# Kernel tuning notes

Hardware: AMD Instinct MI355X
Metric: run time of the kernel (lower is better)

## Reference

```python
import jax, jax.numpy as jnp
import numpy as np

B, T, D = 2, 2048, 1024
NH, DH = 16, 64
DD_PAIRS = DH // 4          # 16
DD_DIM = DD_PAIRS * 2      # 32
FFN = (D * 8 // 3 + 7) // 8 * 8  # 2736
EPS = 1e-6


def rms_norm(x, w):
    # torch nn.RMSNorm: x / sqrt(mean(x^2) + eps) * w over last dim
    var = jnp.mean(jnp.square(x), axis=-1, keepdims=True)
    return x * jax.lax.rsqrt(var + EPS) * w


def apply_rotary(x, cos, sin):
    d = x.shape[-1]
    x1, x2 = x[..., : d // 2], x[..., d // 2 :]
    return jnp.concatenate([x1 * cos - x2 * sin, x2 * cos + x1 * sin], axis=-1)


def setup_inputs() -> dict:
    key = jax.random.key(0)
    ks = jax.random.split(key, 10)
    s = 0.02  # small init scale so activations stay sane
    # fixed RoPE tables: (1, T, 1, DH//2)
    inv_freq = 1.0 / (10000.0 ** (jnp.arange(DH // 2, dtype=jnp.float32) / (DH // 2)))
    ang = jnp.arange(T, dtype=jnp.float32)[:, None] * inv_freq[None, :]  # (T, 32)
    rope_cos = jnp.cos(ang)[None, :, None, :]
    rope_sin = jnp.sin(ang)[None, :, None, :]
    return {
        "x": jax.random.normal(ks[0], (B, T, D), jnp.float32),
        "rope_cos": rope_cos,
        "rope_sin": rope_sin,
        "lerp_w": jax.random.normal(ks[1], (D, D), jnp.float32) * s,
        "lerp_b": jnp.full((D,), -2.0, jnp.float32),
        "attn_norm_w": jnp.ones((D,), jnp.float32),
        "w_qkv": jax.random.normal(ks[2], (3 * D, D), jnp.float32) * s,
        "q_norm_w": jnp.ones((DH,), jnp.float32),
        "k_norm_w": jnp.ones((DH,), jnp.float32),
        "q_post_bias": jnp.ones((DH,), jnp.float32),
        "k_post_bias": jnp.ones((DH,), jnp.float32),
        "dd_w": jax.random.normal(ks[3], (NH * DD_PAIRS, D), jnp.float32) * s,
        "dd_b": jnp.zeros((NH * DD_PAIRS,), jnp.float32),
        "w_o": jax.random.normal(ks[4], (D, D), jnp.float32) * s,
        "mlp_norm_w": jnp.ones((D,), jnp.float32),
        "gate_w": jax.random.normal(ks[5], (FFN, D), jnp.float32) * s,
        "up_w": jax.random.normal(ks[6], (FFN, D), jnp.float32) * s,
        "down_w": jax.random.normal(ks[7], (D, FFN), jnp.float32) * s,
    }


def reference(x, rope_cos, rope_sin, lerp_w, lerp_b, attn_norm_w, w_qkv,
              q_norm_w, k_norm_w, q_post_bias, k_post_bias, dd_w, dd_b,
              w_o, mlp_norm_w, gate_w, up_w, down_w):
    # CausalLerp: x[t] <- (1-g)*x[t] + g*x[t-1], content-gated
    x_prev = jnp.pad(x[:, :-1], ((0, 0), (1, 0), (0, 0)))
    g = jax.nn.sigmoid(x @ lerp_w.T + lerp_b)
    x = (1.0 - g) * x + g * x_prev

    # Attention branch
    h = rms_norm(x, attn_norm_w)
    qkv = (h @ w_qkv.T).reshape(B, T, 3, NH, DH)
    q, k, v = qkv[:, :, 0], qkv[:, :, 1], qkv[:, :, 2]  # (B,T,NH,DH)
    q = rms_norm(q, q_norm_w) * q_post_bias
    k = rms_norm(k, k_norm_w) * k_post_bias

    # DD-RoPE angles: cumsum of learned deltas over time
    dd_angles = (x @ dd_w.T + dd_b).reshape(B, T, NH, DD_PAIRS)
    dd_angles = jnp.cumsum(dd_angles, axis=1)
    dd_cos, dd_sin = jnp.cos(dd_angles), jnp.sin(dd_angles)

    fp = DD_DIM // 2  # 16
    def hybrid(qk):
        fixed = apply_rotary(qk[..., :DD_DIM], rope_cos[..., :fp], rope_sin[..., :fp])
        dd = apply_rotary(qk[..., DD_DIM:], dd_cos, dd_sin)
        return jnp.concatenate([fixed, dd], axis=-1)

    q, k = hybrid(q), hybrid(k)

    # causal SDPA
    scale = 1.0 / jnp.sqrt(jnp.float32(DH))
    scores = jnp.einsum("bihd,bjhd->bhij", q, k) * scale  # (B,NH,T,T)
    causal = jnp.tril(jnp.ones((T, T), bool))
    scores = jnp.where(causal, scores, jnp.float32(-1e30))
    attn = jax.nn.softmax(scores, axis=-1)
    y = jnp.einsum("bhij,bjhd->bihd", attn, v).reshape(B, T, D)
    x = x + y @ w_o.T

    # SwiGLU MLP
    h = rms_norm(x, mlp_norm_w)
    x = x + (jax.nn.silu(h @ gate_w.T) * (h @ up_w.T)) @ down_w.T
    return x
```

## Files before the change

### kernel.cpp

```cpp
#include <hip/hip_runtime.h>

typedef unsigned short u16;
typedef __attribute__((ext_vector_type(8))) short short8;
typedef __attribute__((ext_vector_type(4))) float f32x4;
typedef __attribute__((ext_vector_type(4))) unsigned short u16x4;

static constexpr int TB   = 2;
static constexpr int TT   = 2048;
static constexpr int TD   = 1024;
static constexpr int TNH  = 16;
static constexpr int TDH  = 64;
static constexpr int TFFN = 2736;
static constexpr int TFFNP= 2752;
static constexpr int TBT  = TB * TT;

#define DEVI static __device__ __forceinline__

typedef __attribute__((address_space(1))) const unsigned int gas_t;
typedef __attribute__((address_space(3))) unsigned int las_t;
#define GLOAD16(src, dst) __builtin_amdgcn_global_load_lds((gas_t*)(src), (las_t*)(dst), 16, 0, 0)

DEVI u16 f2bf(float f) {
  union { float f; unsigned u; } v; v.f = f;
  unsigned r = v.u + 0x7FFFu + ((v.u >> 16) & 1u);
  return (u16)(r >> 16);
}
DEVI float bf2f(u16 u) {
  union { unsigned u; float f; } v; v.u = ((unsigned)u) << 16;
  return v.f;
}

__global__ void k_cvt(const float* __restrict__ s, u16* __restrict__ d, int n4) {
  int i = blockIdx.x * blockDim.x + threadIdx.x;
  int st = gridDim.x * blockDim.x;
  for (; i < n4; i += st) {
    float4 v = ((const float4*)s)[i];
    u16x4 u;
    u.x = f2bf(v.x); u.y = f2bf(v.y); u.z = f2bf(v.z); u.w = f2bf(v.w);
    ((u16x4*)d)[i] = u;
  }
}

__global__ void k_cvt_split(const float* __restrict__ s, u16* __restrict__ hi,
                            u16* __restrict__ lo, int n) {
  int i = blockIdx.x * blockDim.x + threadIdx.x;
  int st = gridDim.x * blockDim.x;
  for (; i < n; i += st) {
    float v = s[i];
    u16 h = f2bf(v);
    hi[i] = h;
    lo[i] = f2bf(v - bf2f(h));
  }
}

__global__ void k_cvt_pad(const float* __restrict__ s, u16* __restrict__ d,
                          int rows, int scol, int dcol) {
  int i = blockIdx.x * blockDim.x + threadIdx.x;
  int st = gridDim.x * blockDim.x;
  int n = rows * dcol;
  for (; i < n; i += st) {
    int c = i % dcol, r = i / dcol;
    d[i] = (c < scol) ? f2bf(s[(size_t)r * scol + c]) : (u16)0;
  }
}

__global__ __launch_bounds__(256) void k_rmsnorm(const float* __restrict__ x,
                                                 const float* __restrict__ w,
                                                 u16* __restrict__ o) {
  int row = blockIdx.x;
  float4 v = ((const float4*)(x + (size_t)row * TD))[threadIdx.x];
  float ss = v.x*v.x + v.y*v.y + v.z*v.z + v.w*v.w;
  #pragma unroll
  for (int m = 1; m < 64; m <<= 1) ss += __shfl_xor(ss, m);
  __shared__ float red[4];
  if ((threadIdx.x & 63) == 0) red[threadIdx.x >> 6] = ss;
  __syncthreads();
  float tot = red[0] + red[1] + red[2] + red[3];
  float sc = rsqrtf(tot * (1.0f / TD) + 1e-6f);
  float4 wv = ((const float4*)w)[threadIdx.x];
  u16x4 u;
  u.x = f2bf(v.x * sc * wv.x); u.y = f2bf(v.y * sc * wv.y);
  u.z = f2bf(v.z * sc * wv.z); u.w = f2bf(v.w * sc * wv.w);
  ((u16x4*)(o + (size_t)row * TD))[threadIdx.x] = u;
}

enum { EPI_LERP = 0, EPI_DD = 1, EPI_RESID = 2, EPI_B16 = 3 };

template<int EPI>
__global__ __launch_bounds__(256) void k_gemm_p4(
    const u16* __restrict__ A, const u16* __restrict__ B,
    int M, int N, int K,
    const float* __restrict__ aux0, const float* __restrict__ aux1,
    float* __restrict__ outF, u16* __restrict__ outB) {
  alignas(16) __shared__ u16 As[4][4096];
  alignas(16) __shared__ u16 Bs[4][4096];
  const int lane = threadIdx.x & 63;
  const int w  = threadIdx.x >> 6;
  const int ln = lane & 15;
  const int g  = lane >> 4;
  const int swz = (ln >> 1) & 3;
  const int m0 = blockIdx.x * 128;
  const int n0 = blockIdx.y * 128;
  const int wm = (w >> 1) * 64;
  const int wn = (w & 1) * 64;

  const f32x4 fz = {0.f, 0.f, 0.f, 0.f};
  f32x4 acc[4][4];
  #pragma unroll
  for (int mi = 0; mi < 4; mi++)
    #pragma unroll
    for (int ni = 0; ni < 4; ni++) acc[mi][ni] = fz;

  const int rsub = lane >> 2;
  const int csrc = (lane & 3) ^ ((lane >> 3) & 3);
  auto stage = [&](int buf, int kt) {
    const int k0 = kt * 32 + csrc * 8;
    #pragma unroll
    for (int i = 0; i < 2; i++) {
      const int u = w + i * 4;
      int ar = m0 + u * 16 + rsub;
      GLOAD16(A + (size_t)ar * K + k0, &As[buf][u * 512]);
      int br = n0 + u * 16 + rsub; if (br > N - 1) br = N - 1;
      GLOAD16(B + (size_t)br * K + k0, &Bs[buf][u * 512]);
    }
  };

  const int nt = K / 32;
  stage(0, 0);
  stage(1, 1);
  for (int t = 0; t < nt; ++t) {
    const int cur = t & 3;
    if (t + 2 < nt) {
      stage((t + 2) & 3, t + 2);
      asm volatile("s_waitcnt vmcnt(8)" ::: "memory");
    } else if (t + 1 < nt) {
      asm volatile("s_waitcnt vmcnt(4)" ::: "memory");
    } else {
      asm volatile("s_waitcnt vmcnt(0)" ::: "memory");
    }
    __builtin_amdgcn_s_barrier();
    asm volatile("" ::: "memory");

    short8 af[4], bfr[4];
    #pragma unroll
    for (int mi = 0; mi < 4; mi++)
      af[mi] = *(const short8*)&As[cur][(wm + mi * 16 + ln) * 32 + ((g ^ swz) << 3)];
    #pragma unroll
    for (int ni = 0; ni < 4; ni++)
      bfr[ni] = *(const short8*)&Bs[cur][(wn + ni * 16 + ln) * 32 + ((g ^ swz) << 3)];
    #pragma unroll
    for (int mi = 0; mi < 4; mi++)
      #pragma unroll
      for (int ni = 0; ni < 4; ni++)
        acc[mi][ni] = __builtin_amdgcn_mfma_f32_16x16x32_bf16(af[mi], bfr[ni], acc[mi][ni], 0, 0, 0);
  }

  #pragma unroll
  for (int mi = 0; mi < 4; mi++) {
    #pragma unroll
    for (int ni = 0; ni < 4; ni++) {
      int col = n0 + wn + ni * 16 + ln;
      #pragma unroll
      for (int r = 0; r < 4; r++) {
        int row = m0 + wm + mi * 16 + g * 4 + r;
        if (row >= M || col >= N) continue;
        float c = acc[mi][ni][r];
        size_t o = (size_t)row * N + col;
        if constexpr (EPI == EPI_LERP) {
          float gg = 1.0f / (1.0f + __expf(-(c + aux1[col])));
          float xv = aux0[o];
          float xp = (row & (TT - 1)) ? aux0[o - N] : 0.0f;
          outF[o] = xv + gg * (xp - xv);
        } else if constexpr (EPI == EPI_RESID) {
          outF[o] = aux0[o] + c;
        } else {
          outB[o] = f2bf(c);
        }
      }
    }
  }
}

template<int FM>
__global__ __launch_bounds__(256) void k_gemm_dd(
    const u16* __restrict__ A, const u16* __restrict__ Al,
    const u16* __restrict__ B, const u16* __restrict__ Bl,
    int M, int N, int K, const float* __restrict__ bias,
    float* __restrict__ outF) {
  const int ln = threadIdx.x & 15;
  const int g  = (threadIdx.x >> 4) & 3;
  const int w  = threadIdx.x >> 6;
  const int m0 = blockIdx.x * (FM * 32) + (w >> 1) * (FM * 16);
  const int n0 = blockIdx.y * 128 + (w & 1) * 64;
  size_t aoff[FM], boff[4];
  #pragma unroll
  for (int i = 0; i < FM; i++) {
    int ar = m0 + i * 16 + ln; if (ar > M - 1) ar = M - 1;
    aoff[i] = (size_t)ar * K + g * 8;
  }
  #pragma unroll
  for (int i = 0; i < 4; i++) {
    int br = n0 + i * 16 + ln; if (br > N - 1) br = N - 1;
    boff[i] = (size_t)br * K + g * 8;
  }
  const f32x4 fz = {0.f, 0.f, 0.f, 0.f};
  f32x4 acc[FM][4];
  #pragma unroll
  for (int mi = 0; mi < FM; mi++)
    #pragma unroll
    for (int ni = 0; ni < 4; ni++) acc[mi][ni] = fz;
  for (int k0 = 0; k0 < K; k0 += 32) {
    short8 af[FM], bf[4], al[FM], bl[4];
    #pragma unroll
    for (int i = 0; i < FM; i++) af[i] = *(const short8*)(A + aoff[i] + k0);
    #pragma unroll
    for (int i = 0; i < 4; i++) bf[i] = *(const short8*)(B + boff[i] + k0);
    #pragma unroll
    for (int i = 0; i < FM; i++) al[i] = *(const short8*)(Al + aoff[i] + k0);
    #pragma unroll
    for (int i = 0; i < 4; i++) bl[i] = *(const short8*)(Bl + boff[i] + k0);
    #pragma unroll
    for (int mi = 0; mi < FM; mi++)
      #pragma unroll
      for (int ni = 0; ni < 4; ni++) {
        acc[mi][ni] = __builtin_amdgcn_mfma_f32_16x16x32_bf16(af[mi], bf[ni], acc[mi][ni], 0, 0, 0);
        acc[mi][ni] = __builtin_amdgcn_mfma_f32_16x16x32_bf16(af[mi], bl[ni], acc[mi][ni], 0, 0, 0);
        acc[mi][ni] = __builtin_amdgcn_mfma_f32_16x16x32_bf16(al[mi], bf[ni], acc[mi][ni], 0, 0, 0);
      }
  }
  #pragma unroll
  for (int mi = 0; mi < FM; mi++)
    #pragma unroll
    for (int ni = 0; ni < 4; ni++) {
      int col = n0 + ni * 16 + ln;
      #pragma unroll
      for (int r = 0; r < 4; r++) {
        int row = m0 + mi * 16 + g * 4 + r;
        if (row >= M || col >= N) continue;
        outF[(size_t)row * N + col] = acc[mi][ni][r] + bias[col];
      }
    }
}

__global__ __launch_bounds__(256) void k_cumsum(const float* __restrict__ ang,
                                                float* __restrict__ dc,
                                                float* __restrict__ ds) {
  int col = blockIdx.x & 255;
  int b   = blockIdx.x >> 8;
  int t0  = threadIdx.x * 8;
  size_t base = (size_t)b * TT * 256 + col;
  float v[8];
  #pragma unroll
  for (int i = 0; i < 8; i++) v[i] = ang[base + (size_t)(t0 + i) * 256];
  #pragma unroll
  for (int i = 1; i < 8; i++) v[i] += v[i - 1];
  __shared__ float tot[256];
  tot[threadIdx.x] = v[7];
  __syncthreads();
  for (int o = 1; o < 256; o <<= 1) {
    float a = (threadIdx.x >= o) ? tot[threadIdx.x - o] : 0.0f;
    __syncthreads();
    tot[threadIdx.x] += a;
    __syncthreads();
  }
  float bs = threadIdx.x ? tot[threadIdx.x - 1] : 0.0f;
  #pragma unroll
  for (int i = 0; i < 8; i++) {
    float a = v[i] + bs;
    size_t o = base + (size_t)(t0 + i) * 256;
    dc[o] = cosf(a);
    ds[o] = sinf(a);
  }
}

__global__ __launch_bounds__(64) void k_qkv_post(
    const u16* __restrict__ qkv, const float* __restrict__ rc, const float* __restrict__ rs,
    const float* __restrict__ ddc, const float* __restrict__ dds,
    const float* __restrict__ qnw, const float* __restrict__ knw,
    const float* __restrict__ qpb, const float* __restrict__ kpb,
    u16* __restrict__ qb, u16* __restrict__ kb, u16* __restrict__ vT) {
  int blk = blockIdx.x;
  int h = blk & 15;
  int row = blk >> 4;
  int t = row & (TT - 1);
  int b = row >> 11;
  int d = threadIdx.x;
  size_t base = (size_t)row * (3 * TD) + h * TDH + d;
  float q = bf2f(qkv[base]);
  float k = bf2f(qkv[base + TD]);
  float v = bf2f(qkv[base + 2 * TD]);
  float sq = q * q, sk = k * k;
  #pragma unroll
  for (int m = 1; m < 64; m <<= 1) { sq += __shfl_xor(sq, m); sk += __shfl_xor(sk, m); }
  q *= rsqrtf(sq * (1.0f / TDH) + 1e-6f) * qnw[d] * qpb[d];
  k *= rsqrtf(sk * (1.0f / TDH) + 1e-6f) * knw[d] * kpb[d];
  float c, s;
  if (d < 32) {
    c = rc[t * 32 + (d & 15)];
    s = rs[t * 32 + (d & 15)];
  } else {
    size_t ti = (size_t)row * 256 + h * 16 + (d & 15);
    c = ddc[ti];
    s = dds[ti];
  }
  float oq = __shfl_xor(q, 16);
  float ok = __shfl_xor(k, 16);
  float sgn = (d & 16) ? 1.0f : -1.0f;
  float qr = q * c + sgn * oq * s;
  float kr = k * c + sgn * ok * s;
  qr *= 0.125f;
  int bh = b * TNH + h;
  size_t o = ((size_t)bh * TT + t) * TDH + d;
  qb[o] = f2bf(qr);
  kb[o] = f2bf(kr);
  vT[((size_t)bh * TDH + d) * TT + t] = f2bf(v);
}

__global__ __launch_bounds__(256) void k_attn(
    const u16* __restrict__ qb, const u16* __restrict__ kb,
    const u16* __restrict__ vT, u16* __restrict__ y) {
  __shared__ u16 Ks[2][4096];
  __shared__ u16 Vs[2][4096];
  __shared__ u16 plds[4][16][80];
  const int lane = threadIdx.x & 63;
  const int w = threadIdx.x >> 6;
  const int ln = lane & 15;
  const int g = lane >> 4;
  const int bh = blockIdx.x;
  const int b = bh >> 4, h = bh & 15;
  const int by = 31 - (int)blockIdx.y;
  const int qt0 = by * 64 + w * 16;
  const u16* Q  = qb + (size_t)bh * TT * TDH;
  const u16* Kp = kb + (size_t)bh * TT * TDH;
  const u16* Vp = vT + (size_t)bh * TDH * TT;
  short8 qa0 = *(const short8*)(Q + (size_t)(qt0 + ln) * TDH + g * 8);
  short8 qa1 = *(const short8*)(Q + (size_t)(qt0 + ln) * TDH + 32 + g * 8);
  const f32x4 fz = {0.f, 0.f, 0.f, 0.f};
  f32x4 O[4];
  float mrow[4], lrow[4];
  #pragma unroll
  for (int r = 0; r < 4; r++) { O[r] = fz; mrow[r] = -1e30f; lrow[r] = 0.0f; }

  auto stage = [&](int buf, int j0) {
    #pragma unroll
    for (int i = 0; i < 2; i++) {
      int r = w * 16 + i * 8 + (lane >> 3);
      int c = (lane & 7) ^ (r & 7);
      GLOAD16(Kp + (size_t)(j0 + r) * TDH + c * 8, &Ks[buf][w * 1024 + i * 512]);
      GLOAD16(Vp + (size_t)r * TT + j0 + c * 8, &Vs[buf][w * 1024 + i * 512]);
    }
  };

  const int nt = by + 1;
  stage(0, 0);
  __syncthreads();
  for (int jt = 0; jt < nt; ++jt) {
    const int cur = jt & 1;
    if (jt + 1 < nt) stage(cur ^ 1, (jt + 1) * 64);
    const int j0 = jt * 64;
    f32x4 sc[4];
    #pragma unroll
    for (int c4 = 0; c4 < 4; c4++) {
      int j = c4 * 16 + ln;
      const u16* kr = &Ks[cur][j * 64];
      short8 k0 = *(const short8*)(kr + ((g ^ (j & 7)) * 8));
      short8 k1 = *(const short8*)(kr + (((g + 4) ^ (j & 7)) * 8));
      f32x4 z = fz;
      z = __builtin_amdgcn_mfma_f32_16x16x32_bf16(qa0, k0, z, 0, 0, 0);
      z = __builtin_amdgcn_mfma_f32_16x16x32_bf16(qa1, k1, z, 0, 0, 0);
      sc[c4] = z;
    }
    if (jt == nt - 1) {
      #pragma unroll
      for (int c4 = 0; c4 < 4; c4++)
        #pragma unroll
        for (int r = 0; r < 4; r++)
          if (j0 + c4 * 16 + ln > qt0 + g * 4 + r) sc[c4][r] = -1e30f;
    }
    float mn[4], corr[4], rsum[4];
    #pragma unroll
    for (int r = 0; r < 4; r++) {
      float mv = fmaxf(fmaxf(sc[0][r], sc[1][r]), fmaxf(sc[2][r], sc[3][r]));
      #pragma unroll
      for (int mm = 1; mm < 16; mm <<= 1) mv = fmaxf(mv, __shfl_xor(mv, mm));
      mn[r] = fmaxf(mrow[r], mv);
      corr[r] = __expf(mrow[r] - mn[r]);
      rsum[r] = 0.0f;
    }
    #pragma unroll
    for (int c4 = 0; c4 < 4; c4++)
      #pragma unroll
      for (int r = 0; r < 4; r++) {
        float p = __expf(sc[c4][r] - mn[r]);
        rsum[r] += p;
        plds[w][g * 4 + r][c4 * 16 + ln] = f2bf(p);
      }
    #pragma unroll
    for (int r = 0; r < 4; r++) {
      float t = rsum[r];
      #pragma unroll
      for (int mm = 1; mm < 16; mm <<= 1) t += __shfl_xor(t, mm);
      lrow[r] = lrow[r] * corr[r] + t;
      mrow[r] = mn[r];
    }
    #pragma unroll
    for (int dc = 0; dc < 4; dc++)
      #pragma unroll
      for (int r = 0; r < 4; r++) O[dc][r] *= corr[r];
    short8 pa0 = *(const short8*)&plds[w][ln][g * 8];
    short8 pa1 = *(const short8*)&plds[w][ln][32 + g * 8];
    #pragma unroll
    for (int dc = 0; dc < 4; dc++) {
      int dd = dc * 16 + ln;
      const u16* vr = &Vs[cur][dd * 64];
      short8 v0 = *(const short8*)(vr + ((g ^ (dd & 7)) * 8));
      short8 v1 = *(const short8*)(vr + (((g + 4) ^ (dd & 7)) * 8));
      O[dc] = __builtin_amdgcn_mfma_f32_16x16x32_bf16(pa0, v0, O[dc], 0, 0, 0);
      O[dc] = __builtin_amdgcn_mfma_f32_16x16x32_bf16(pa1, v1, O[dc], 0, 0, 0);
    }
    __syncthreads();
  }
  #pragma unroll
  for (int r = 0; r < 4; r++) {
    int t = qt0 + g * 4 + r;
    float inv = 1.0f / lrow[r];
    size_t o = ((size_t)(b * TT + t)) * TD + h * TDH;
    #pragma unroll
    for (int dc = 0; dc < 4; dc++)
      y[o + dc * 16 + ln] = f2bf(O[dc][r] * inv);
  }
}

__global__ void k_swiglu(const u16* __restrict__ gb, const u16* __restrict__ ub,
                         u16* __restrict__ hb) {
  int i = blockIdx.x * blockDim.x + threadIdx.x;
  int st = gridDim.x * blockDim.x;
  int n = TBT * TFFNP;
  for (; i < n; i += st) {
    int c = i % TFFNP;
    int r = i / TFFNP;
    u16 o = 0;
    if (c < TFFN) {
      float gv = bf2f(gb[(size_t)r * TFFN + c]);
      float uv = bf2f(ub[(size_t)r * TFFN + c]);
      float sg = gv / (1.0f + __expf(-gv));
      o = f2bf(sg * uv);
    }
    hb[i] = o;
  }
}

extern "C" void kernel_launch(void* const* d_in, const int* in_sizes, int n_in,
                              void* d_out, int out_size, void* d_ws, size_t ws_size,
                              hipStream_t stream) {
  const float* x      = (const float*)d_in[0];
  const float* ropec  = (const float*)d_in[1];
  const float* ropes  = (const float*)d_in[2];
  const float* lerp_w = (const float*)d_in[3];
  const float* lerp_b = (const float*)d_in[4];
  const float* anw    = (const float*)d_in[5];
  const float* w_qkv  = (const float*)d_in[6];
  const float* qnw    = (const float*)d_in[7];
  const float* knw    = (const float*)d_in[8];
  const float* qpb    = (const float*)d_in[9];
  const float* kpb    = (const float*)d_in[10];
  const float* dd_w   = (const float*)d_in[11];
  const float* dd_b   = (const float*)d_in[12];
  const float* w_o    = (const float*)d_in[13];
  const float* mnw    = (const float*)d_in[14];
  const float* gate_w = (const float*)d_in[15];
  const float* up_w   = (const float*)d_in[16];
  const float* down_w = (const float*)d_in[17];
  float* out = (float*)d_out;
  (void)in_sizes; (void)n_in; (void)out_size; (void)ws_size;

  char* ws = (char*)d_ws;
  size_t off = 0;
  auto alloc = [&](size_t bytes) -> char* {
    char* p = ws + off;
    off += (bytes + 255) & ~(size_t)255;
    return p;
  };

  char* seg1 = ws;
  u16* xb      = (u16*)alloc((size_t)TBT * TD * 2);
  u16* wb_lerp = (u16*)alloc((size_t)TD * TD * 2);
  u16* wb_qkv  = (u16*)alloc((size_t)3 * TD * TD * 2);
  u16* h_b     = (u16*)alloc((size_t)TBT * TD * 2);
  u16* hb      = (u16*)seg1;

  u16* wdd_h   = (u16*)alloc((size_t)256 * TD * 2);
  u16* wdd_l   = (u16*)alloc((size_t)256 * TD * 2);
  u16* wb_o    = (u16*)alloc((size_t)TD * TD * 2);
  u16* wb_gate = (u16*)alloc((size_t)TFFN * TD * 2);
  u16* wb_up   = (u16*)alloc((size_t)TFFN * TD * 2);
  u16* wb_down = (u16*)alloc((size_t)TD * TFFNP * 2);
  float* x_mix = (float*)alloc((size_t)TBT * TD * 4);

  char* seg4 = ws + off;
  u16* xh      = (u16*)alloc((size_t)TBT * TD * 2);
  u16* xl      = (u16*)alloc((size_t)TBT * TD * 2);
  float* angles= (float*)alloc((size_t)TBT * 256 * 4);
  float* ddc   = (float*)alloc((size_t)TBT * 256 * 4);
  float* dds   = (float*)alloc((size_t)TBT * 256 * 4);
  u16* up_b    = (u16*)seg4;

  char* seg5 = ws + off;
  u16* qkv_b   = (u16*)alloc((size_t)TBT * 3 * TD * 2);
  u16* gate_b  = (u16*)seg5;

  u16* qb  = (u16*)alloc((size_t)TBT * TD * 2);
  u16* kb  = (u16*)alloc((size_t)TBT * TD * 2);
  u16* vT  = (u16*)alloc((size_t)TBT * TD * 2);
  u16* y_b = (u16*)alloc((size_t)TBT * TD * 2);
  float* x2  = (float*)alloc((size_t)TBT * TD * 4);
  u16* h2_b  = (u16*)alloc((size_t)TBT * TD * 2);

  k_cvt<<<dim3(1024), dim3(256), 0, stream>>>(x, xb, TBT * TD / 4);
  k_cvt<<<dim3(256),  dim3(256), 0, stream>>>(lerp_w, wb_lerp, TD * TD / 4);
  k_cvt<<<dim3(768),  dim3(256), 0, stream>>>(w_qkv, wb_qkv, 3 * TD * TD / 4);
  k_cvt_split<<<dim3(256), dim3(256), 0, stream>>>(dd_w, wdd_h, wdd_l, 256 * TD);
  k_cvt<<<dim3(256),  dim3(256), 0, stream>>>(w_o, wb_o, TD * TD / 4);
  k_cvt<<<dim3(512),  dim3(256), 0, stream>>>(gate_w, wb_gate, TFFN * TD / 4);
  k_cvt<<<dim3(512),  dim3(256), 0, stream>>>(up_w, wb_up, TFFN * TD / 4);
  k_cvt_pad<<<dim3(512), dim3(256), 0, stream>>>(down_w, wb_down, TD, TFFN, TFFNP);

  k_gemm_p4<EPI_LERP><<<dim3(32, 8), dim3(256), 0, stream>>>(
      xb, wb_lerp, TBT, TD, TD, x, lerp_b, x_mix, nullptr);

  k_cvt_split<<<dim3(1024), dim3(256), 0, stream>>>(x_mix, xh, xl, TBT * TD);
  k_rmsnorm<<<dim3(TBT), dim3(256), 0, stream>>>(x_mix, anw, h_b);

  k_gemm_p4<EPI_B16><<<dim3(32, 24), dim3(256), 0, stream>>>(
      h_b, wb_qkv, TBT, 3 * TD, TD, nullptr, nullptr, nullptr, qkv_b);

  k_gemm_dd<2><<<dim3(64, 2), dim3(256), 0, stream>>>(
      xh, xl, wdd_h, wdd_l, TBT, 256, TD, dd_b, angles);

  k_cumsum<<<dim3(512), dim3(256), 0, stream>>>(angles, ddc, dds);

  k_qkv_post<<<dim3(TBT * TNH), dim3(64), 0, stream>>>(
      qkv_b, ropec, ropes, ddc, dds, qnw, knw, qpb, kpb, qb, kb, vT);

  k_attn<<<dim3(32, 32), dim3(256), 0, stream>>>(qb, kb, vT, y_b);

  k_gemm_p4<EPI_RESID><<<dim3(32, 8), dim3(256), 0, stream>>>(
      y_b, wb_o, TBT, TD, TD, x_mix, nullptr, x2, nullptr);

  k_rmsnorm<<<dim3(TBT), dim3(256), 0, stream>>>(x2, mnw, h2_b);
  k_gemm_p4<EPI_B16><<<dim3(32, 22), dim3(256), 0, stream>>>(
      h2_b, wb_gate, TBT, TFFN, TD, nullptr, nullptr, nullptr, gate_b);
  k_gemm_p4<EPI_B16><<<dim3(32, 22), dim3(256), 0, stream>>>(
      h2_b, wb_up, TBT, TFFN, TD, nullptr, nullptr, nullptr, up_b);
  k_swiglu<<<dim3(2048), dim3(256), 0, stream>>>(gate_b, up_b, hb);
  k_gemm_p4<EPI_RESID><<<dim3(32, 8), dim3(256), 0, stream>>>(
      hb, wb_down, TBT, TD, TFFNP, x2, nullptr, out, nullptr);
}
```

Measured before the change: 628.5 us.

## Fuse gate/up GEMMs, fold split-precision DD into concatenated-K GEMM, rework attention and cumsum

Gate and up projections are merged into one GEMM over concatenated weights, and the swiglu kernel reads the combined output with 8-wide vector loads. The hi/lo split-precision DD GEMM becomes a single bf16 GEMM over a K=3072 concatenation, whose A operand is written directly by the lerp epilogue. The cumsum is split into a three-pass segmented scan. qkv_post now handles 64 tokens per block and transposes V through LDS for coalesced writes. Attention keeps P in registers via swapped MFMA operands and 16x16x16 MFMAs instead of an LDS round trip, and stages its output for coalesced stores. Together these cut launches, memory traffic and LDS usage, at the cost of more complex indexing and a larger DD GEMM.

```diff
diff --git a/kernel.cpp b/kernel.cpp
--- a/kernel.cpp
+++ b/kernel.cpp
@@ -2,6 +2,7 @@
 
 typedef unsigned short u16;
 typedef __attribute__((ext_vector_type(8))) short short8;
+typedef __attribute__((ext_vector_type(4))) short short4v;
 typedef __attribute__((ext_vector_type(4))) float f32x4;
 typedef __attribute__((ext_vector_type(4))) unsigned short u16x4;
 
@@ -30,6 +31,22 @@
   return v.f;
 }
 
+DEVI unsigned cvtpk(float lo, float hi) {
+  unsigned r;
+  asm("v_cvt_pk_bf16_f32 %0, %1, %2" : "=v"(r) : "v"(lo), "v"(hi));
+  return r;
+}
+
+#if __has_builtin(__builtin_amdgcn_mfma_f32_16x16x16bf16_1k)
+#define MFMA16(a, b, c) __builtin_amdgcn_mfma_f32_16x16x16bf16_1k(a, b, c, 0, 0, 0)
+#else
+DEVI f32x4 mfma16_asm(short4v a, short4v b, f32x4 c) {
+  asm("v_mfma_f32_16x16x16_bf16 %0, %1, %2, %0" : "+v"(c) : "v"(a), "v"(b));
+  return c;
+}
+#define MFMA16(a, b, c) mfma16_asm(a, b, c)
+#endif
+
 __global__ void k_cvt(const float* __restrict__ s, u16* __restrict__ d, int n4) {
   int i = blockIdx.x * blockDim.x + threadIdx.x;
   int st = gridDim.x * blockDim.x;
@@ -41,15 +58,17 @@
   }
 }
 
-__global__ void k_cvt_split(const float* __restrict__ s, u16* __restrict__ hi,
-                            u16* __restrict__ lo, int n) {
+__global__ void k_cvt_split3(const float* __restrict__ s, u16* __restrict__ d, int n) {
   int i = blockIdx.x * blockDim.x + threadIdx.x;
   int st = gridDim.x * blockDim.x;
   for (; i < n; i += st) {
+    int c = i & 1023, r = i >> 10;
     float v = s[i];
     u16 h = f2bf(v);
-    hi[i] = h;
-    lo[i] = f2bf(v - bf2f(h));
+    size_t base = (size_t)r * 3072 + c;
+    d[base] = h;
+    d[base + 1024] = h;
+    d[base + 2048] = f2bf(v - bf2f(h));
   }
 }
 
@@ -86,28 +105,29 @@
 
 enum { EPI_LERP = 0, EPI_DD = 1, EPI_RESID = 2, EPI_B16 = 3 };
 
-template<int EPI>
+template<int BM, int EPI>
 __global__ __launch_bounds__(256) void k_gemm_p4(
     const u16* __restrict__ A, const u16* __restrict__ B,
     int M, int N, int K,
     const float* __restrict__ aux0, const float* __restrict__ aux1,
     float* __restrict__ outF, u16* __restrict__ outB) {
-  alignas(16) __shared__ u16 As[4][4096];
+  constexpr int MI = BM / 32;
+  alignas(16) __shared__ u16 As[4][BM * 32];
   alignas(16) __shared__ u16 Bs[4][4096];
   const int lane = threadIdx.x & 63;
   const int w  = threadIdx.x >> 6;
   const int ln = lane & 15;
   const int g  = lane >> 4;
   const int swz = (ln >> 1) & 3;
-  const int m0 = blockIdx.x * 128;
+  const int m0 = blockIdx.x * BM;
   const int n0 = blockIdx.y * 128;
-  const int wm = (w >> 1) * 64;
+  const int wm = (w >> 1) * (BM / 2);
   const int wn = (w & 1) * 64;
 
   const f32x4 fz = {0.f, 0.f, 0.f, 0.f};
-  f32x4 acc[4][4];
+  f32x4 acc[MI][4];
   #pragma unroll
-  for (int mi = 0; mi < 4; mi++)
+  for (int mi = 0; mi < MI; mi++)
     #pragma unroll
     for (int ni = 0; ni < 4; ni++) acc[mi][ni] = fz;
 
@@ -115,13 +135,24 @@
   const int csrc = (lane & 3) ^ ((lane >> 3) & 3);
   auto stage = [&](int buf, int kt) {
     const int k0 = kt * 32 + csrc * 8;
-    #pragma unroll
-    for (int i = 0; i < 2; i++) {
-      const int u = w + i * 4;
-      int ar = m0 + u * 16 + rsub;
-      GLOAD16(A + (size_t)ar * K + k0, &As[buf][u * 512]);
-      int br = n0 + u * 16 + rsub; if (br > N - 1) br = N - 1;
-      GLOAD16(B + (size_t)br * K + k0, &Bs[buf][u * 512]);
+    if constexpr (BM == 128) {
+      #pragma unroll
+      for (int i = 0; i < 2; i++) {
+        const int u = w + i * 4;
+        int ar = m0 + u * 16 + rsub;
+        GLOAD16(A + (size_t)ar * K + k0, &As[buf][u * 512]);
+        int br = n0 + u * 16 + rsub; if (br > N - 1) br = N - 1;
+        GLOAD16(B + (size_t)br * K + k0, &Bs[buf][u * 512]);
+      }
+    } else {
+      int ar = m0 + w * 16 + rsub;
+      GLOAD16(A + (size_t)ar * K + k0, &As[buf][w * 512]);
+      #pragma unroll
+      for (int i = 0; i < 2; i++) {
+        const int u = w + i * 4;
+        int br = n0 + u * 16 + rsub; if (br > N - 1) br = N - 1;
+        GLOAD16(B + (size_t)br * K + k0, &Bs[buf][u * 512]);
+      }
     }
   };
 
@@ -132,31 +163,33 @@
     const int cur = t & 3;
     if (t + 2 < nt) {
       stage((t + 2) & 3, t + 2);
-      asm volatile("s_waitcnt vmcnt(8)" ::: "memory");
+      if constexpr (BM == 128) asm volatile("s_waitcnt vmcnt(8)" ::: "memory");
+      else                     asm volatile("s_waitcnt vmcnt(6)" ::: "memory");
     } else if (t + 1 < nt) {
-      asm volatile("s_waitcnt vmcnt(4)" ::: "memory");
+      if constexpr (BM == 128) asm volatile("s_waitcnt vmcnt(4)" ::: "memory");
+      else                     asm volatile("s_waitcnt vmcnt(3)" ::: "memory");
     } else {
       asm volatile("s_waitcnt vmcnt(0)" ::: "memory");
     }
     __builtin_amdgcn_s_barrier();
     asm volatile("" ::: "memory");
 
-    short8 af[4], bfr[4];
-    #pragma unroll
-    for (int mi = 0; mi < 4; mi++)
+    short8 af[MI], bfr[4];
+    #pragma unroll
+    for (int mi = 0; mi < MI; mi++)
       af[mi] = *(const short8*)&As[cur][(wm + mi * 16 + ln) * 32 + ((g ^ swz) << 3)];
     #pragma unroll
     for (int ni = 0; ni < 4; ni++)
       bfr[ni] = *(const short8*)&Bs[cur][(wn + ni * 16 + ln) * 32 + ((g ^ swz) << 3)];
     #pragma unroll
-    for (int mi = 0; mi < 4; mi++)
+    for (int mi = 0; mi < MI; mi++)
       #pragma unroll
       for (int ni = 0; ni < 4; ni++)
         acc[mi][ni] = __builtin_amdgcn_mfma_f32_16x16x32_bf16(af[mi], bfr[ni], acc[mi][ni], 0, 0, 0);
   }
 
   #pragma unroll
-  for (int mi = 0; mi < 4; mi++) {
+  for (int mi = 0; mi < MI; mi++) {
     #pragma unroll
     for (int ni = 0; ni < 4; ni++) {
       int col = n0 + wn + ni * 16 + ln;
@@ -170,7 +203,15 @@
           float gg = 1.0f / (1.0f + __expf(-(c + aux1[col])));
           float xv = aux0[o];
           float xp = (row & (TT - 1)) ? aux0[o - N] : 0.0f;
-          outF[o] = xv + gg * (xp - xv);
+          float res = xv + gg * (xp - xv);
+          outF[o] = res;
+          u16 hi = f2bf(res);
+          size_t xc = (size_t)row * 3072 + col;
+          outB[xc] = hi;
+          outB[xc + 2048] = hi;
+          outB[xc + 1024] = f2bf(res - bf2f(hi));
+        } else if constexpr (EPI == EPI_DD) {
+          outF[o] = c + aux1[col];
         } else if constexpr (EPI == EPI_RESID) {
           outF[o] = aux0[o] + c;
         } else {
@@ -181,153 +222,119 @@
   }
 }
 
-template<int FM>
-__global__ __launch_bounds__(256) void k_gemm_dd(
-    const u16* __restrict__ A, const u16* __restrict__ Al,
-    const u16* __restrict__ B, const u16* __restrict__ Bl,
-    int M, int N, int K, const float* __restrict__ bias,
-    float* __restrict__ outF) {
-  const int ln = threadIdx.x & 15;
-  const int g  = (threadIdx.x >> 4) & 3;
-  const int w  = threadIdx.x >> 6;
-  const int m0 = blockIdx.x * (FM * 32) + (w >> 1) * (FM * 16);
-  const int n0 = blockIdx.y * 128 + (w & 1) * 64;
-  size_t aoff[FM], boff[4];
-  #pragma unroll
-  for (int i = 0; i < FM; i++) {
-    int ar = m0 + i * 16 + ln; if (ar > M - 1) ar = M - 1;
-    aoff[i] = (size_t)ar * K + g * 8;
-  }
-  #pragma unroll
-  for (int i = 0; i < 4; i++) {
-    int br = n0 + i * 16 + ln; if (br > N - 1) br = N - 1;
-    boff[i] = (size_t)br * K + g * 8;
-  }
-  const f32x4 fz = {0.f, 0.f, 0.f, 0.f};
-  f32x4 acc[FM][4];
-  #pragma unroll
-  for (int mi = 0; mi < FM; mi++)
-    #pragma unroll
-    for (int ni = 0; ni < 4; ni++) acc[mi][ni] = fz;
-  for (int k0 = 0; k0 < K; k0 += 32) {
-    short8 af[FM], bf[4], al[FM], bl[4];
-    #pragma unroll
-    for (int i = 0; i < FM; i++) af[i] = *(const short8*)(A + aoff[i] + k0);
-    #pragma unroll
-    for (int i = 0; i < 4; i++) bf[i] = *(const short8*)(B + boff[i] + k0);
-    #pragma unroll
-    for (int i = 0; i < FM; i++) al[i] = *(const short8*)(Al + aoff[i] + k0);
-    #pragma unroll
-    for (int i = 0; i < 4; i++) bl[i] = *(const short8*)(Bl + boff[i] + k0);
-    #pragma unroll
-    for (int mi = 0; mi < FM; mi++)
-      #pragma unroll
-      for (int ni = 0; ni < 4; ni++) {
-        acc[mi][ni] = __builtin_amdgcn_mfma_f32_16x16x32_bf16(af[mi], bf[ni], acc[mi][ni], 0, 0, 0);
-        acc[mi][ni] = __builtin_amdgcn_mfma_f32_16x16x32_bf16(af[mi], bl[ni], acc[mi][ni], 0, 0, 0);
-        acc[mi][ni] = __builtin_amdgcn_mfma_f32_16x16x32_bf16(al[mi], bf[ni], acc[mi][ni], 0, 0, 0);
-      }
-  }
-  #pragma unroll
-  for (int mi = 0; mi < FM; mi++)
-    #pragma unroll
-    for (int ni = 0; ni < 4; ni++) {
-      int col = n0 + ni * 16 + ln;
-      #pragma unroll
-      for (int r = 0; r < 4; r++) {
-        int row = m0 + mi * 16 + g * 4 + r;
-        if (row >= M || col >= N) continue;
-        outF[(size_t)row * N + col] = acc[mi][ni][r] + bias[col];
-      }
-    }
-}
-
-__global__ __launch_bounds__(256) void k_cumsum(const float* __restrict__ ang,
-                                                float* __restrict__ dc,
-                                                float* __restrict__ ds) {
-  int col = blockIdx.x & 255;
-  int b   = blockIdx.x >> 8;
-  int t0  = threadIdx.x * 8;
-  size_t base = (size_t)b * TT * 256 + col;
-  float v[8];
-  #pragma unroll
-  for (int i = 0; i < 8; i++) v[i] = ang[base + (size_t)(t0 + i) * 256];
-  #pragma unroll
-  for (int i = 1; i < 8; i++) v[i] += v[i - 1];
-  __shared__ float tot[256];
-  tot[threadIdx.x] = v[7];
-  __syncthreads();
-  for (int o = 1; o < 256; o <<= 1) {
-    float a = (threadIdx.x >= o) ? tot[threadIdx.x - o] : 0.0f;
-    __syncthreads();
-    tot[threadIdx.x] += a;
-    __syncthreads();
-  }
-  float bs = threadIdx.x ? tot[threadIdx.x - 1] : 0.0f;
-  #pragma unroll
-  for (int i = 0; i < 8; i++) {
-    float a = v[i] + bs;
-    size_t o = base + (size_t)(t0 + i) * 256;
-    dc[o] = cosf(a);
-    ds[o] = sinf(a);
-  }
-}
-
-__global__ __launch_bounds__(64) void k_qkv_post(
+__global__ __launch_bounds__(64) void k_csum1(const float* __restrict__ ang,
+                                              float* __restrict__ seg) {
+  int b = blockIdx.x, sg = blockIdx.y, q = threadIdx.x;
+  const float4* p = (const float4*)(ang + ((size_t)(b * TT + sg * 16)) * 256) + q;
+  float4 a = {0.f, 0.f, 0.f, 0.f};
+  #pragma unroll 4
+  for (int i = 0; i < 16; i++) {
+    float4 v = p[(size_t)i * 64];
+    a.x += v.x; a.y += v.y; a.z += v.z; a.w += v.w;
+  }
+  ((float4*)(seg + ((size_t)(b * 128 + sg)) * 256))[q] = a;
+}
+
+__global__ __launch_bounds__(512) void k_csum2(float* __restrict__ seg) {
+  int b = threadIdx.x >> 8, col = threadIdx.x & 255;
+  float acc = 0.f;
+  for (int s = 0; s < 128; s++) {
+    size_t o = ((size_t)(b * 128 + s)) * 256 + col;
+    float v = seg[o];
+    seg[o] = acc;
+    acc += v;
+  }
+}
+
+__global__ __launch_bounds__(64) void k_csum3(const float* __restrict__ ang,
+                                              const float* __restrict__ seg,
+                                              float* __restrict__ dc,
+                                              float* __restrict__ ds) {
+  int b = blockIdx.x, sg = blockIdx.y, q = threadIdx.x;
+  size_t rowbase = ((size_t)(b * TT + sg * 16)) * 256;
+  const float4* p = (const float4*)(ang + rowbase) + q;
+  float4 a = ((const float4*)(seg + ((size_t)(b * 128 + sg)) * 256))[q];
+  for (int i = 0; i < 16; i++) {
+    float4 v = p[(size_t)i * 64];
+    a.x += v.x; a.y += v.y; a.z += v.z; a.w += v.w;
+    float4 c, s;
+    c.x = cosf(a.x); s.x = sinf(a.x);
+    c.y = cosf(a.y); s.y = sinf(a.y);
+    c.z = cosf(a.z); s.z = sinf(a.z);
+    c.w = cosf(a.w); s.w = sinf(a.w);
+    ((float4*)(dc + rowbase))[(size_t)i * 64 + q] = c;
+    ((float4*)(ds + rowbase))[(size_t)i * 64 + q] = s;
+  }
+}
+
+__global__ __launch_bounds__(256) void k_qkv_post(
     const u16* __restrict__ qkv, const float* __restrict__ rc, const float* __restrict__ rs,
     const float* __restrict__ ddc, const float* __restrict__ dds,
     const float* __restrict__ qnw, const float* __restrict__ knw,
     const float* __restrict__ qpb, const float* __restrict__ kpb,
     u16* __restrict__ qb, u16* __restrict__ kb, u16* __restrict__ vT) {
-  int blk = blockIdx.x;
-  int h = blk & 15;
-  int row = blk >> 4;
-  int t = row & (TT - 1);
-  int b = row >> 11;
-  int d = threadIdx.x;
-  size_t base = (size_t)row * (3 * TD) + h * TDH + d;
-  float q = bf2f(qkv[base]);
-  float k = bf2f(qkv[base + TD]);
-  float v = bf2f(qkv[base + 2 * TD]);
-  float sq = q * q, sk = k * k;
-  #pragma unroll
-  for (int m = 1; m < 64; m <<= 1) { sq += __shfl_xor(sq, m); sk += __shfl_xor(sk, m); }
-  q *= rsqrtf(sq * (1.0f / TDH) + 1e-6f) * qnw[d] * qpb[d];
-  k *= rsqrtf(sk * (1.0f / TDH) + 1e-6f) * knw[d] * kpb[d];
-  float c, s;
-  if (d < 32) {
-    c = rc[t * 32 + (d & 15)];
-    s = rs[t * 32 + (d & 15)];
-  } else {
-    size_t ti = (size_t)row * 256 + h * 16 + (d & 15);
-    c = ddc[ti];
-    s = dds[ti];
-  }
-  float oq = __shfl_xor(q, 16);
-  float ok = __shfl_xor(k, 16);
-  float sgn = (d & 16) ? 1.0f : -1.0f;
-  float qr = q * c + sgn * oq * s;
-  float kr = k * c + sgn * ok * s;
-  qr *= 0.125f;
-  int bh = b * TNH + h;
-  size_t o = ((size_t)bh * TT + t) * TDH + d;
-  qb[o] = f2bf(qr);
-  kb[o] = f2bf(kr);
-  vT[((size_t)bh * TDH + d) * TT + t] = f2bf(v);
+  __shared__ u16 vt[64][72];
+  const int lane = threadIdx.x & 63;
+  const int w = threadIdx.x >> 6;
+  const int bh = blockIdx.x, b = bh >> 4, h = bh & 15;
+  const int t0 = blockIdx.y * 64;
+  const float qsc = 0.125f * 1.44269504f;
+  const float qw = qnw[lane] * qpb[lane];
+  const float kw = knw[lane] * kpb[lane];
+  const float sgn = (lane & 16) ? 1.0f : -1.0f;
+  #pragma unroll 4
+  for (int it = 0; it < 16; ++it) {
+    int tl = w * 16 + it;
+    int t = t0 + tl;
+    size_t base = ((size_t)(b * TT + t)) * 3072 + h * 64 + lane;
+    float q = bf2f(qkv[base]);
+    float k = bf2f(qkv[base + 1024]);
+    float v = bf2f(qkv[base + 2048]);
+    float sq = q * q, sk = k * k;
+    #pragma unroll
+    for (int m = 1; m < 64; m <<= 1) { sq += __shfl_xor(sq, m); sk += __shfl_xor(sk, m); }
+    q *= rsqrtf(sq * (1.0f / TDH) + 1e-6f) * qw;
+    k *= rsqrtf(sk * (1.0f / TDH) + 1e-6f) * kw;
+    float c, s;
+    if (lane < 32) {
+      c = rc[t * 32 + (lane & 15)];
+      s = rs[t * 32 + (lane & 15)];
+    } else {
+      size_t ti = ((size_t)(b * TT + t)) * 256 + h * 16 + (lane & 15);
+      c = ddc[ti];
+      s = dds[ti];
+    }
+    float oq = __shfl_xor(q, 16);
+    float ok = __shfl_xor(k, 16);
+    float qr = (q * c + sgn * oq * s) * qsc;
+    float kr = k * c + sgn * ok * s;
+    size_t o = ((size_t)(bh * TT + t)) * 64 + lane;
+    qb[o] = f2bf(qr);
+    kb[o] = f2bf(kr);
+    vt[lane][tl] = f2bf(v);
+  }
+  __syncthreads();
+  int row = threadIdx.x >> 2, sg = threadIdx.x & 3;
+  short8 v0 = *(const short8*)&vt[row][sg * 16];
+  short8 v1 = *(const short8*)&vt[row][sg * 16 + 8];
+  size_t o = ((size_t)(bh * 64 + row)) * TT + t0 + sg * 16;
+  *(short8*)(vT + o) = v0;
+  *(short8*)(vT + o + 8) = v1;
 }
 
 __global__ __launch_bounds__(256) void k_attn(
     const u16* __restrict__ qb, const u16* __restrict__ kb,
     const u16* __restrict__ vT, u16* __restrict__ y) {
-  __shared__ u16 Ks[2][4096];
-  __shared__ u16 Vs[2][4096];
-  __shared__ u16 plds[4][16][80];
+  __shared__ u16 smem[16384];
+  u16* Ks = smem;
+  u16* Vs = smem + 8192;
   const int lane = threadIdx.x & 63;
   const int w = threadIdx.x >> 6;
   const int ln = lane & 15;
   const int g = lane >> 4;
+  const int gh = g >> 1, gl = g & 1;
   const int bh = blockIdx.x;
-  const int b = bh >> 4, h = bh & 15;
+  const int b = bh >> 4;
   const int by = 31 - (int)blockIdx.y;
   const int qt0 = by * 64 + w * 16;
   const u16* Q  = qb + (size_t)bh * TT * TDH;
@@ -337,17 +344,18 @@
   short8 qa1 = *(const short8*)(Q + (size_t)(qt0 + ln) * TDH + 32 + g * 8);
   const f32x4 fz = {0.f, 0.f, 0.f, 0.f};
   f32x4 O[4];
-  float mrow[4], lrow[4];
   #pragma unroll
-  for (int r = 0; r < 4; r++) { O[r] = fz; mrow[r] = -1e30f; lrow[r] = 0.0f; }
+  for (int r = 0; r < 4; r++) O[r] = fz;
+  float m = -1e30f, l = 0.0f;
+  const int qlim = qt0 + ln;
 
   auto stage = [&](int buf, int j0) {
     #pragma unroll
     for (int i = 0; i < 2; i++) {
       int r = w * 16 + i * 8 + (lane >> 3);
       int c = (lane & 7) ^ (r & 7);
-      GLOAD16(Kp + (size_t)(j0 + r) * TDH + c * 8, &Ks[buf][w * 1024 + i * 512]);
-      GLOAD16(Vp + (size_t)r * TT + j0 + c * 8, &Vs[buf][w * 1024 + i * 512]);
+      GLOAD16(Kp + (size_t)(j0 + r) * TDH + c * 8, &Ks[buf * 4096 + w * 1024 + i * 512]);
+      GLOAD16(Vp + (size_t)r * TT + j0 + c * 8, &Vs[buf * 4096 + w * 1024 + i * 512]);
     }
   };
 
@@ -361,13 +369,12 @@
     f32x4 sc[4];
     #pragma unroll
     for (int c4 = 0; c4 < 4; c4++) {
-      int j = c4 * 16 + ln;
-      const u16* kr = &Ks[cur][j * 64];
-      short8 k0 = *(const short8*)(kr + ((g ^ (j & 7)) * 8));
-      short8 k1 = *(const short8*)(kr + (((g + 4) ^ (j & 7)) * 8));
+      const u16* kr = Ks + cur * 4096 + (c4 * 16 + ln) * 64;
+      short8 k0 = *(const short8*)(kr + ((g ^ (ln & 7)) * 8));
+      short8 k1 = *(const short8*)(kr + (((g + 4) ^ (ln & 7)) * 8));
       f32x4 z = fz;
-      z = __builtin_amdgcn_mfma_f32_16x16x32_bf16(qa0, k0, z, 0, 0, 0);
-      z = __builtin_amdgcn_mfma_f32_16x16x32_bf16(qa1, k1, z, 0, 0, 0);
+      z = __builtin_amdgcn_mfma_f32_16x16x32_bf16(k0, qa0, z, 0, 0, 0);
+      z = __builtin_amdgcn_mfma_f32_16x16x32_bf16(k1, qa1, z, 0, 0, 0);
       sc[c4] = z;
     }
     if (jt == nt - 1) {
@@ -375,79 +382,99 @@
       for (int c4 = 0; c4 < 4; c4++)
         #pragma unroll
         for (int r = 0; r < 4; r++)
-          if (j0 + c4 * 16 + ln > qt0 + g * 4 + r) sc[c4][r] = -1e30f;
-    }
-    float mn[4], corr[4], rsum[4];
-    #pragma unroll
-    for (int r = 0; r < 4; r++) {
-      float mv = fmaxf(fmaxf(sc[0][r], sc[1][r]), fmaxf(sc[2][r], sc[3][r]));
-      #pragma unroll
-      for (int mm = 1; mm < 16; mm <<= 1) mv = fmaxf(mv, __shfl_xor(mv, mm));
-      mn[r] = fmaxf(mrow[r], mv);
-      corr[r] = __expf(mrow[r] - mn[r]);
-      rsum[r] = 0.0f;
-    }
+          if (j0 + c4 * 16 + g * 4 + r > qlim) sc[c4][r] = -1e30f;
+    }
+    float pm = sc[0][0];
     #pragma unroll
     for (int c4 = 0; c4 < 4; c4++)
       #pragma unroll
+      for (int r = 0; r < 4; r++) pm = fmaxf(pm, sc[c4][r]);
+    pm = fmaxf(pm, __shfl_xor(pm, 16));
+    pm = fmaxf(pm, __shfl_xor(pm, 32));
+    bool grow = pm > m + 10.0f;
+    if (__ballot(grow) != 0ull) {
+      float mn = fmaxf(m, pm);
+      float corr = exp2f(m - mn);
+      #pragma unroll
+      for (int dc = 0; dc < 4; dc++)
+        #pragma unroll
+        for (int r = 0; r < 4; r++) O[dc][r] *= corr;
+      l *= corr;
+      m = mn;
+    }
+    float rs_ = 0.0f;
+    #pragma unroll
+    for (int c4 = 0; c4 < 4; c4++)
+      #pragma unroll
       for (int r = 0; r < 4; r++) {
-        float p = __expf(sc[c4][r] - mn[r]);
-        rsum[r] += p;
-        plds[w][g * 4 + r][c4 * 16 + ln] = f2bf(p);
+        float pv = exp2f(sc[c4][r] - m);
+        rs_ += pv;
+        sc[c4][r] = pv;
       }
-    #pragma unroll
-    for (int r = 0; r < 4; r++) {
-      float t = rsum[r];
-      #pragma unroll
-      for (int mm = 1; mm < 16; mm <<= 1) t += __shfl_xor(t, mm);
-      lrow[r] = lrow[r] * corr[r] + t;
-      mrow[r] = mn[r];
-    }
-    #pragma unroll
-    for (int dc = 0; dc < 4; dc++)
-      #pragma unroll
-      for (int r = 0; r < 4; r++) O[dc][r] *= corr[r];
-    short8 pa0 = *(const short8*)&plds[w][ln][g * 8];
-    short8 pa1 = *(const short8*)&plds[w][ln][32 + g * 8];
+    rs_ += __shfl_xor(rs_, 16);
+    rs_ += __shfl_xor(rs_, 32);
+    l += rs_;
+    short4v p4[4];
+    #pragma unroll
+    for (int c4 = 0; c4 < 4; c4++) {
+      union { unsigned u[2]; short4v s; } pu;
+      pu.u[0] = cvtpk(sc[c4][0], sc[c4][1]);
+      pu.u[1] = cvtpk(sc[c4][2], sc[c4][3]);
+      p4[c4] = pu.s;
+    }
     #pragma unroll
     for (int dc = 0; dc < 4; dc++) {
-      int dd = dc * 16 + ln;
-      const u16* vr = &Vs[cur][dd * 64];
-      short8 v0 = *(const short8*)(vr + ((g ^ (dd & 7)) * 8));
-      short8 v1 = *(const short8*)(vr + (((g + 4) ^ (dd & 7)) * 8));
-      O[dc] = __builtin_amdgcn_mfma_f32_16x16x32_bf16(pa0, v0, O[dc], 0, 0, 0);
-      O[dc] = __builtin_amdgcn_mfma_f32_16x16x32_bf16(pa1, v1, O[dc], 0, 0, 0);
+      const int vrow = dc * 16 + ln;
+      const u16* vbase = Vs + cur * 4096 + vrow * 64;
+      #pragma unroll
+      for (int c4 = 0; c4 < 4; c4++) {
+        int chunk = (2 * c4 + gh) ^ (ln & 7);
+        short4v va = *(const short4v*)(vbase + chunk * 8 + gl * 4);
+        O[dc] = MFMA16(va, p4[c4], O[dc]);
+      }
     }
     __syncthreads();
   }
+  u16* ot = smem + w * 1152;
+  float inv = 1.0f / l;
   #pragma unroll
-  for (int r = 0; r < 4; r++) {
-    int t = qt0 + g * 4 + r;
-    float inv = 1.0f / lrow[r];
-    size_t o = ((size_t)(b * TT + t)) * TD + h * TDH;
-    #pragma unroll
-    for (int dc = 0; dc < 4; dc++)
-      y[o + dc * 16 + ln] = f2bf(O[dc][r] * inv);
-  }
-}
-
-__global__ void k_swiglu(const u16* __restrict__ gb, const u16* __restrict__ ub,
-                         u16* __restrict__ hb) {
+  for (int dc = 0; dc < 4; dc++)
+    #pragma unroll
+    for (int r = 0; r < 4; r += 2) {
+      unsigned pk = cvtpk(O[dc][r] * inv, O[dc][r + 1] * inv);
+      *(unsigned*)(ot + ln * 72 + dc * 16 + g * 4 + r) = pk;
+    }
+  __syncthreads();
+  int row = (threadIdx.x & 63) >> 2, sg = threadIdx.x & 3;
+  u16* os = smem + w * 1152;
+  short8 v0 = *(const short8*)(os + row * 72 + sg * 16);
+  short8 v1 = *(const short8*)(os + row * 72 + sg * 16 + 8);
+  size_t o = ((size_t)(b * TT + qt0 + row)) * TD + (bh & 15) * TDH + sg * 16;
+  *(short8*)(y + o) = v0;
+  *(short8*)(y + o + 8) = v1;
+}
+
+__global__ void k_swiglu(const u16* __restrict__ gu, u16* __restrict__ hb) {
   int i = blockIdx.x * blockDim.x + threadIdx.x;
-  int st = gridDim.x * blockDim.x;
-  int n = TBT * TFFNP;
-  for (; i < n; i += st) {
-    int c = i % TFFNP;
-    int r = i / TFFNP;
-    u16 o = 0;
-    if (c < TFFN) {
-      float gv = bf2f(gb[(size_t)r * TFFN + c]);
-      float uv = bf2f(ub[(size_t)r * TFFN + c]);
-      float sg = gv / (1.0f + __expf(-gv));
-      o = f2bf(sg * uv);
-    }
-    hb[i] = o;
-  }
+  int n = TBT * 344;
+  if (i >= n) return;
+  int c8 = i % 344, r = i / 344;
+  short8 o;
+  if (c8 < 342) {
+    short8 gv = *(const short8*)(gu + (size_t)r * 5472 + c8 * 8);
+    short8 uv = *(const short8*)(gu + (size_t)r * 5472 + 2736 + c8 * 8);
+    #pragma unroll
+    for (int j = 0; j < 8; j++) {
+      float gf = bf2f((u16)gv[j]);
+      float uf = bf2f((u16)uv[j]);
+      float sg = gf / (1.0f + __expf(-gf));
+      o[j] = (short)f2bf(sg * uf);
+    }
+  } else {
+    #pragma unroll
+    for (int j = 0; j < 8; j++) o[j] = 0;
+  }
+  *(short8*)(hb + (size_t)r * TFFNP + c8 * 8) = o;
 }
 
 extern "C" void kernel_launch(void* const* d_in, const int* in_sizes, int n_in,
@@ -482,33 +509,27 @@
     return p;
   };
 
-  char* seg1 = ws;
+  char* segA = ws;
   u16* xb      = (u16*)alloc((size_t)TBT * TD * 2);
   u16* wb_lerp = (u16*)alloc((size_t)TD * TD * 2);
   u16* wb_qkv  = (u16*)alloc((size_t)3 * TD * TD * 2);
   u16* h_b     = (u16*)alloc((size_t)TBT * TD * 2);
-  u16* hb      = (u16*)seg1;
-
-  u16* wdd_h   = (u16*)alloc((size_t)256 * TD * 2);
-  u16* wdd_l   = (u16*)alloc((size_t)256 * TD * 2);
+  u16* xcat    = (u16*)alloc((size_t)TBT * 3072 * 2);
+  u16* gu_b    = (u16*)segA;
+
+  char* segF = ws + off;
+  u16* qkv_b   = (u16*)alloc((size_t)TBT * 3 * TD * 2);
+  u16* hb      = (u16*)segF;
+
+  u16* wcat    = (u16*)alloc((size_t)256 * 3072 * 2);
   u16* wb_o    = (u16*)alloc((size_t)TD * TD * 2);
-  u16* wb_gate = (u16*)alloc((size_t)TFFN * TD * 2);
-  u16* wb_up   = (u16*)alloc((size_t)TFFN * TD * 2);
+  u16* wb_gu   = (u16*)alloc((size_t)2 * TFFN * TD * 2);
   u16* wb_down = (u16*)alloc((size_t)TD * TFFNP * 2);
   float* x_mix = (float*)alloc((size_t)TBT * TD * 4);
-
-  char* seg4 = ws + off;
-  u16* xh      = (u16*)alloc((size_t)TBT * TD * 2);
-  u16* xl      = (u16*)alloc((size_t)TBT * TD * 2);
   float* angles= (float*)alloc((size_t)TBT * 256 * 4);
   float* ddc   = (float*)alloc((size_t)TBT * 256 * 4);
   float* dds   = (float*)alloc((size_t)TBT * 256 * 4);
-  u16* up_b    = (u16*)seg4;
-
-  char* seg5 = ws + off;
-  u16* qkv_b   = (u16*)alloc((size_t)TBT * 3 * TD * 2);
-  u16* gate_b  = (u16*)seg5;
-
+  float* segsum= (float*)alloc((size_t)2 * 128 * 256 * 4);
   u16* qb  = (u16*)alloc((size_t)TBT * TD * 2);
   u16* kb  = (u16*)alloc((size_t)TBT * TD * 2);
   u16* vT  = (u16*)alloc((size_t)TBT * TD * 2);
@@ -519,40 +540,39 @@
   k_cvt<<<dim3(1024), dim3(256), 0, stream>>>(x, xb, TBT * TD / 4);
   k_cvt<<<dim3(256),  dim3(256), 0, stream>>>(lerp_w, wb_lerp, TD * TD / 4);
   k_cvt<<<dim3(768),  dim3(256), 0, stream>>>(w_qkv, wb_qkv, 3 * TD * TD / 4);
-  k_cvt_split<<<dim3(256), dim3(256), 0, stream>>>(dd_w, wdd_h, wdd_l, 256 * TD);
+  k_cvt_split3<<<dim3(256), dim3(256), 0, stream>>>(dd_w, wcat, 256 * TD);
   k_cvt<<<dim3(256),  dim3(256), 0, stream>>>(w_o, wb_o, TD * TD / 4);
-  k_cvt<<<dim3(512),  dim3(256), 0, stream>>>(gate_w, wb_gate, TFFN * TD / 4);
-  k_cvt<<<dim3(512),  dim3(256), 0, stream>>>(up_w, wb_up, TFFN * TD / 4);
+  k_cvt<<<dim3(512),  dim3(256), 0, stream>>>(gate_w, wb_gu, TFFN * TD / 4);
+  k_cvt<<<dim3(512),  dim3(256), 0, stream>>>(up_w, wb_gu + (size_t)TFFN * TD, TFFN * TD / 4);
   k_cvt_pad<<<dim3(512), dim3(256), 0, stream>>>(down_w, wb_down, TD, TFFN, TFFNP);
 
-  k_gemm_p4<EPI_LERP><<<dim3(32, 8), dim3(256), 0, stream>>>(
-      xb, wb_lerp, TBT, TD, TD, x, lerp_b, x_mix, nullptr);
-
-  k_cvt_split<<<dim3(1024), dim3(256), 0, stream>>>(x_mix, xh, xl, TBT * TD);
+  k_gemm_p4<128, EPI_LERP><<<dim3(32, 8), dim3(256), 0, stream>>>(
+      xb, wb_lerp, TBT, TD, TD, x, lerp_b, x_mix, xcat);
+
   k_rmsnorm<<<dim3(TBT), dim3(256), 0, stream>>>(x_mix, anw, h_b);
 
-  k_gemm_p4<EPI_B16><<<dim3(32, 24), dim3(256), 0, stream>>>(
+  k_gemm_p4<128, EPI_B16><<<dim3(32, 24), dim3(256), 0, stream>>>(
       h_b, wb_qkv, TBT, 3 * TD, TD, nullptr, nullptr, nullptr, qkv_b);
 
-  k_gemm_dd<2><<<dim3(64, 2), dim3(256), 0, stream>>>(
-      xh, xl, wdd_h, wdd_l, TBT, 256, TD, dd_b, angles);
-
-  k_cumsum<<<dim3(512), dim3(256), 0, stream>>>(angles, ddc, dds);
-
-  k_qkv_post<<<dim3(TBT * TNH), dim3(64), 0, stream>>>(
+  k_gemm_p4<64, EPI_DD><<<dim3(64, 2), dim3(256), 0, stream>>>(
+      xcat, wcat, TBT, 256, 3072, nullptr, dd_b, angles, nullptr);
+
+  k_csum1<<<dim3(2, 128), dim3(64), 0, stream>>>(angles, segsum);
+  k_csum2<<<dim3(1), dim3(512), 0, stream>>>(segsum);
+  k_csum3<<<dim3(2, 128), dim3(64), 0, stream>>>(angles, segsum, ddc, dds);
+
+  k_qkv_post<<<dim3(32, 32), dim3(256), 0, stream>>>(
       qkv_b, ropec, ropes, ddc, dds, qnw, knw, qpb, kpb, qb, kb, vT);
 
   k_attn<<<dim3(32, 32), dim3(256), 0, stream>>>(qb, kb, vT, y_b);
 
-  k_gemm_p4<EPI_RESID><<<dim3(32, 8), dim3(256), 0, stream>>>(
+  k_gemm_p4<128, EPI_RESID><<<dim3(32, 8), dim3(256), 0, stream>>>(
       y_b, wb_o, TBT, TD, TD, x_mix, nullptr, x2, nullptr);
 
   k_rmsnorm<<<dim3(TBT), dim3(256), 0, stream>>>(x2, mnw, h2_b);
-  k_gemm_p4<EPI_B16><<<dim3(32, 22), dim3(256), 0, stream>>>(
-      h2_b, wb_gate, TBT, TFFN, TD, nullptr, nullptr, nullptr, gate_b);
-  k_gemm_p4<EPI_B16><<<dim3(32, 22), dim3(256), 0, stream>>>(
-      h2_b, wb_up, TBT, TFFN, TD, nullptr, nullptr, nullptr, up_b);
-  k_swiglu<<<dim3(2048), dim3(256), 0, stream>>>(gate_b, up_b, hb);
-  k_gemm_p4<EPI_RESID><<<dim3(32, 8), dim3(256), 0, stream>>>(
+  k_gemm_p4<128, EPI_B16><<<dim3(32, 43), dim3(256), 0, stream>>>(
+      h2_b, wb_gu, TBT, 2 * TFFN, TD, nullptr, nullptr, nullptr, gu_b);
+  k_swiglu<<<dim3((TBT * 344 + 255) / 256), dim3(256), 0, stream>>>(gu_b, hb);
+  k_gemm_p4<128, EPI_RESID><<<dim3(32, 8), dim3(256), 0, stream>>>(
       hb, wb_down, TBT, TD, TFFNP, x2, nullptr, out, nullptr);
 }
```

Result: faster. 570.5 us (-9.2%).
